# Kernel optimization log

Measured on AMD Instinct MI355X. Metric: run time of the kernel, lower is better.

The kernel has to match this reference:

```python
import jax, jax.numpy as jnp
import numpy as np

NUM_RANKS = 8   # tp_group.size()
M = 8192        # global token dim (batch*seq), M % (256*NUM_RANKS) == 0
N = 4096        # output features
K_LOCAL = 512   # per-rank shard of the contracted dim (global K = 4096)


def setup_inputs() -> dict:
    key = jax.random.key(0)
    k1, k2 = jax.random.split(key)
    # a[r] = this rank's input shard [M, K_local]
    a = jax.random.normal(k1, (NUM_RANKS, M, K_LOCAL), dtype=jnp.float32)
    # b[r] = this rank's weight shard [N, K_local]; GEMM is input @ weight.T
    b = jax.random.normal(k2, (NUM_RANKS, N, K_LOCAL), dtype=jnp.float32)
    return {"a": a, "b": b}


def reference(a, b):
    # Simulates gemm_rs_intra_node across all ranks.
    # Per-rank GEMM (non-transposed weight path: C_r = a_r @ b_r^T)
    R, M_, _ = a.shape
    N_ = b.shape[1]
    m_per_rank = M_ // R
    partial = jnp.einsum('rmk,rnk->rmn', a, b)  # [R, M, N] partial products
    # Reduce-scatter over the M dim: out[r] = sum_src partial[src, r*mpr:(r+1)*mpr, :]
    # (the fused scatter writes each M-chunk into the owning rank's buffer,
    #  kernel_consumer_reduce then sums over source ranks)
    out = partial.reshape(R, R, m_per_rank, N_).sum(axis=0)  # sum over source ranks
    return out  # [R, M_per_rank, N]
```

## Files before the change

kernel.cpp:

```cpp
#include <hip/hip_runtime.h>
#include <hip/hip_bf16.h>
#include <stdint.h>

#define NUM_RANKS 8
#define M_DIM 8192
#define N_DIM 4096
#define K_LOC 512
#define K_DIM 4096
#define NT    (K_DIM / 64)

typedef __bf16 bf16x8 __attribute__((ext_vector_type(8)));
typedef float f32x4 __attribute__((ext_vector_type(4)));

__device__ __forceinline__ uint32_t f2bf(float f) {
    union { float f; uint32_t u; } cv;
    cv.f = f;
    uint32_t x = cv.u;
    return ((x + 0x7fffu + ((x >> 16) & 1u)) >> 16) & 0xffffu;
}

__global__ __launch_bounds__(256) void cvt_fused(
    const float* __restrict__ a, const float* __restrict__ b,
    unsigned short* __restrict__ Abf, unsigned short* __restrict__ Bbf)
{
    const long ACH = (long)NUM_RANKS * M_DIM * (K_LOC / 8);
    const long TCH = ACH + (long)NUM_RANKS * N_DIM * (K_LOC / 8);
    for (long c = (long)blockIdx.x * 256 + threadIdx.x; c < TCH;
         c += (long)gridDim.x * 256) {
        const float* in; unsigned short* out; long e; int rowShift;
        if (c < ACH) { in = a; out = Abf; e = c << 3;        rowShift = 13; }
        else         { in = b; out = Bbf; e = (c - ACH) << 3; rowShift = 12; }
        const int src = (int)(e >> (rowShift + 9));
        const int row = (int)((e >> 9) & ((1 << rowShift) - 1));
        const int k   = (int)(e & 511);
        const float4 f0 = *(const float4*)(in + e);
        const float4 f1 = *(const float4*)(in + e + 4);
        uint4 v;
        v.x = f2bf(f0.x) | (f2bf(f0.y) << 16);
        v.y = f2bf(f0.z) | (f2bf(f0.w) << 16);
        v.z = f2bf(f1.x) | (f2bf(f1.y) << 16);
        v.w = f2bf(f1.z) | (f2bf(f1.w) << 16);
        *(uint4*)(out + ((long)row << 12) + (src << 9) + k) = v;
    }
}

__device__ __forceinline__ void load_lds16(const void* g, void* l) {
    __builtin_amdgcn_global_load_lds(
        (__attribute__((address_space(1))) void*)g,
        (__attribute__((address_space(3))) void*)l,
        16, 0, 0);
}


#define MFMA16 __builtin_amdgcn_mfma_f32_16x16x32_bf16
#define BAR() do { \
    __builtin_amdgcn_sched_barrier(0); \
    asm volatile("s_barrier" ::: "memory"); \
    __builtin_amdgcn_sched_barrier(0); \
} while (0)
#define WAIT_LGKM() do { \
    asm volatile("s_waitcnt lgkmcnt(0)" ::: "memory"); \
    __builtin_amdgcn_sched_barrier(0); \
} while (0)
#define WAIT_VM(n) asm volatile("s_waitcnt vmcnt(" #n ")" ::: "memory")

#define STAGE_A(h, kt, bsel) do { \
    const long kof_ = (long)(kt) * 64; \
    load_lds16(gA0 + (long)((h) * 128) * K_DIM + kof_, \
               lA + (bsel) * 16384 + (h) * 8192); \
    load_lds16(gA0 + (long)((h) * 128 + 64) * K_DIM + kof_, \
               lA + (bsel) * 16384 + (h) * 8192 + 4096); \
} while (0)
#define STAGE_B(h, kt, bsel) do { \
    const long kof_ = (long)(kt) * 64; \
    load_lds16(gB0 + (long)((h) * 128) * K_DIM + kof_, \
               lB + (bsel) * 16384 + (h) * 8192); \
    load_lds16(gB0 + (long)((h) * 128 + 64) * K_DIM + kof_, \
               lB + (bsel) * 16384 + (h) * 8192 + 4096); \
} while (0)

#define READ_A(mh, bsel) do { \
    _Pragma("unroll") \
    for (int mi_ = 0; mi_ < 4; ++mi_) { \
        af[mi_][0] = *(const bf16x8*)(&sA[bsel][baseA0 + ((mh) * 64 + mi_ * 16) * 64]); \
        af[mi_][1] = *(const bf16x8*)(&sA[bsel][baseA1 + ((mh) * 64 + mi_ * 16) * 64]); \
    } \
} while (0)
#define READ_B(nh, bsel) do { \
    _Pragma("unroll") \
    for (int ni_ = 0; ni_ < 2; ++ni_) { \
        bfr[ni_][0] = *(const bf16x8*)(&sB[bsel][baseB0 + ((nh) * 32 + ni_ * 16) * 64]); \
        bfr[ni_][1] = *(const bf16x8*)(&sB[bsel][baseB1 + ((nh) * 32 + ni_ * 16) * 64]); \
    } \
} while (0)

#define DO_MFMA(mh, nh) do { \
    __builtin_amdgcn_s_setprio(1); \
    _Pragma("unroll") \
    for (int mi_ = 0; mi_ < 4; ++mi_) { \
        _Pragma("unroll") \
        for (int ni_ = 0; ni_ < 2; ++ni_) { \
            acc[(mh) * 4 + mi_][(nh) * 2 + ni_] = MFMA16( \
                af[mi_][0], bfr[ni_][0], acc[(mh) * 4 + mi_][(nh) * 2 + ni_], 0, 0, 0); \
            acc[(mh) * 4 + mi_][(nh) * 2 + ni_] = MFMA16( \
                af[mi_][1], bfr[ni_][1], acc[(mh) * 4 + mi_][(nh) * 2 + ni_], 0, 0, 0); \
        } \
    } \
    __builtin_amdgcn_s_setprio(0); \
} while (0)

#define TILE(bsel, kt, sN, sA2, vmend) do { \
    READ_A(0, bsel); READ_B(0, bsel); \
    if (sN) STAGE_A(1, (kt) + 1, (bsel) ^ 1); \
    BAR(); WAIT_LGKM(); DO_MFMA(0, 0); BAR(); \
    READ_B(1, bsel); \
    if (sN) STAGE_B(0, (kt) + 1, (bsel) ^ 1); \
    BAR(); WAIT_LGKM(); DO_MFMA(0, 1); BAR(); \
    READ_A(1, bsel); \
    if (sN) STAGE_B(1, (kt) + 1, (bsel) ^ 1); \
    BAR(); WAIT_LGKM(); DO_MFMA(1, 1); BAR(); \
    READ_B(0, bsel); \
    if (sA2) STAGE_A(0, (kt) + 2, bsel); \
    BAR(); WAIT_LGKM(); DO_MFMA(1, 0); \
    if ((vmend) == 2) { WAIT_VM(2); } \
    else if ((vmend) == 0) { WAIT_VM(0); } \
    BAR(); \
} while (0)

__global__ __launch_bounds__(512, 2) void gemm_bt(
    const unsigned short* __restrict__ A,
    const unsigned short* __restrict__ B,
    float* __restrict__ C)
{
    __shared__ unsigned short sA[2][16384];
    __shared__ unsigned short sB[2][16384];

    const int t    = threadIdx.x;
    const int lane = t & 63;
    const int w    = t >> 6;
    const int wm   = w >> 2;
    const int wn   = w & 3;
    const int l16  = lane & 15;
    const int quad = lane >> 4;

    const int m0 = blockIdx.y << 8;
    const int n0 = blockIdx.x << 8;

    const int r0 = t >> 3;
    const int cs = (((t & 7) ^ ((t >> 3) & 7)) << 3);
    const unsigned short* gA0 = A + (long)(m0 + r0) * K_DIM + cs;
    const unsigned short* gB0 = B + (long)(n0 + r0) * K_DIM + cs;
    unsigned short* lA = &sA[0][t * 8];
    unsigned short* lB = &sB[0][t * 8];

    const int xq = l16 & 7;
    const int baseA0 = ((wm * 128 + l16) << 6) + ((quad ^ xq) << 3);
    const int baseA1 = ((wm * 128 + l16) << 6) + (((4 + quad) ^ xq) << 3);
    const int baseB0 = ((wn * 64 + l16) << 6) + ((quad ^ xq) << 3);
    const int baseB1 = ((wn * 64 + l16) << 6) + (((4 + quad) ^ xq) << 3);

    f32x4 acc[8][4];
#pragma unroll
    for (int i = 0; i < 8; ++i)
#pragma unroll
        for (int j = 0; j < 4; ++j)
            acc[i][j] = (f32x4){0.f, 0.f, 0.f, 0.f};

    bf16x8 af[4][2], bfr[2][2];

    STAGE_A(0, 0, 0); STAGE_A(1, 0, 0); STAGE_B(0, 0, 0); STAGE_B(1, 0, 0);
    STAGE_A(0, 1, 1);
    WAIT_VM(2);
    BAR();

    for (int tt = 0; tt < NT / 2 - 1; ++tt) {
        TILE(0, 2 * tt,     1, 1, 2);
        TILE(1, 2 * tt + 1, 1, 1, 2);
    }
    TILE(0, NT - 2, 1, 0, 0);
    TILE(1, NT - 1, 0, 0, -1);

#pragma unroll
    for (int mi8 = 0; mi8 < 8; ++mi8) {
#pragma unroll
        for (int ni = 0; ni < 4; ++ni) {
            const int col = n0 + wn * 64 + ni * 16 + l16;
            const long rbase = (long)(m0 + wm * 128 + mi8 * 16 + quad * 4);
#pragma unroll
            for (int r = 0; r < 4; ++r)
                C[(rbase + r) * N_DIM + col] = acc[mi8][ni][r];
        }
    }
}

extern "C" void kernel_launch(void* const* d_in, const int* in_sizes, int n_in,
                              void* d_out, int out_size, void* d_ws, size_t ws_size,
                              hipStream_t stream)
{
    const float* a = (const float*)d_in[0];
    const float* b = (const float*)d_in[1];
    float* out = (float*)d_out;

    unsigned short* Abf = (unsigned short*)d_ws;
    unsigned short* Bbf = Abf + (size_t)M_DIM * K_DIM;

    cvt_fused<<<2048, 256, 0, stream>>>(a, b, Abf, Bbf);

    dim3 grid(N_DIM / 256, M_DIM / 256);
    gemm_bt<<<grid, 512, 0, stream>>>(Abf, Bbf, out);
}
```

Baseline: 528.0 us.

## Double-buffer LDS fragment registers and relax waitcnts to overlap reads with MFMA

Restructures the per-tile schedule so LDS fragment reads for the next quarter-tile (and the next tile's first A/B fragments) are issued before the current MFMA block. Waits become partial lgkmcnt counts instead of full drains, and fewer barriers are used. Global-to-LDS staging is reordered so more loads stay in flight, with B staged two tiles ahead. The extra fragment registers raise VGPR pressure, and the reordered stage and barrier timing risks LDS read/write races.

```diff
diff --git a/kernel.cpp b/kernel.cpp
--- a/kernel.cpp
+++ b/kernel.cpp
@@ -58,11 +58,14 @@
     asm volatile("s_barrier" ::: "memory"); \
     __builtin_amdgcn_sched_barrier(0); \
 } while (0)
-#define WAIT_LGKM() do { \
-    asm volatile("s_waitcnt lgkmcnt(0)" ::: "memory"); \
+#define LGKM(n) do { \
+    asm volatile("s_waitcnt lgkmcnt(" #n ")" ::: "memory"); \
     __builtin_amdgcn_sched_barrier(0); \
 } while (0)
-#define WAIT_VM(n) asm volatile("s_waitcnt vmcnt(" #n ")" ::: "memory")
+#define VM_6    asm volatile("s_waitcnt vmcnt(6)" ::: "memory")
+#define VM_2    asm volatile("s_waitcnt vmcnt(2)" ::: "memory")
+#define VM_0    asm volatile("s_waitcnt vmcnt(0)" ::: "memory")
+#define VM_NONE
 
 #define STAGE_A(h, kt, bsel) do { \
     const long kof_ = (long)(kt) * 64; \
@@ -79,51 +82,54 @@
                lB + (bsel) * 16384 + (h) * 8192 + 4096); \
 } while (0)
 
-#define READ_A(mh, bsel) do { \
+#define RD_A(mh, dst, bsel) do { \
     _Pragma("unroll") \
     for (int mi_ = 0; mi_ < 4; ++mi_) { \
-        af[mi_][0] = *(const bf16x8*)(&sA[bsel][baseA0 + ((mh) * 64 + mi_ * 16) * 64]); \
-        af[mi_][1] = *(const bf16x8*)(&sA[bsel][baseA1 + ((mh) * 64 + mi_ * 16) * 64]); \
+        af[dst][mi_][0] = *(const bf16x8*)(&sA[bsel][baseA0 + ((mh) * 64 + mi_ * 16) * 64]); \
+        af[dst][mi_][1] = *(const bf16x8*)(&sA[bsel][baseA1 + ((mh) * 64 + mi_ * 16) * 64]); \
     } \
 } while (0)
-#define READ_B(nh, bsel) do { \
+#define RD_B(nh, dst, bsel) do { \
     _Pragma("unroll") \
     for (int ni_ = 0; ni_ < 2; ++ni_) { \
-        bfr[ni_][0] = *(const bf16x8*)(&sB[bsel][baseB0 + ((nh) * 32 + ni_ * 16) * 64]); \
-        bfr[ni_][1] = *(const bf16x8*)(&sB[bsel][baseB1 + ((nh) * 32 + ni_ * 16) * 64]); \
+        bq[dst][ni_][0] = *(const bf16x8*)(&sB[bsel][baseB0 + ((nh) * 32 + ni_ * 16) * 64]); \
+        bq[dst][ni_][1] = *(const bf16x8*)(&sB[bsel][baseB1 + ((nh) * 32 + ni_ * 16) * 64]); \
     } \
 } while (0)
 
-#define DO_MFMA(mh, nh) do { \
+#define DO_MFMA(mh, nh, aset, bset) do { \
     __builtin_amdgcn_s_setprio(1); \
     _Pragma("unroll") \
     for (int mi_ = 0; mi_ < 4; ++mi_) { \
         _Pragma("unroll") \
         for (int ni_ = 0; ni_ < 2; ++ni_) { \
             acc[(mh) * 4 + mi_][(nh) * 2 + ni_] = MFMA16( \
-                af[mi_][0], bfr[ni_][0], acc[(mh) * 4 + mi_][(nh) * 2 + ni_], 0, 0, 0); \
+                af[aset][mi_][0], bq[bset][ni_][0], \
+                acc[(mh) * 4 + mi_][(nh) * 2 + ni_], 0, 0, 0); \
             acc[(mh) * 4 + mi_][(nh) * 2 + ni_] = MFMA16( \
-                af[mi_][1], bfr[ni_][1], acc[(mh) * 4 + mi_][(nh) * 2 + ni_], 0, 0, 0); \
+                af[aset][mi_][1], bq[bset][ni_][1], \
+                acc[(mh) * 4 + mi_][(nh) * 2 + ni_], 0, 0, 0); \
         } \
     } \
     __builtin_amdgcn_s_setprio(0); \
 } while (0)
 
-#define TILE(bsel, kt, sN, sA2, vmend) do { \
-    READ_A(0, bsel); READ_B(0, bsel); \
-    if (sN) STAGE_A(1, (kt) + 1, (bsel) ^ 1); \
-    BAR(); WAIT_LGKM(); DO_MFMA(0, 0); BAR(); \
-    READ_B(1, bsel); \
-    if (sN) STAGE_B(0, (kt) + 1, (bsel) ^ 1); \
-    BAR(); WAIT_LGKM(); DO_MFMA(0, 1); BAR(); \
-    READ_A(1, bsel); \
-    if (sN) STAGE_B(1, (kt) + 1, (bsel) ^ 1); \
-    BAR(); WAIT_LGKM(); DO_MFMA(1, 1); BAR(); \
-    READ_B(0, bsel); \
-    if (sA2) STAGE_A(0, (kt) + 2, bsel); \
-    BAR(); WAIT_LGKM(); DO_MFMA(1, 0); \
-    if ((vmend) == 2) { WAIT_VM(2); } \
-    else if ((vmend) == 0) { WAIT_VM(0); } \
+#define TILE(bsel, kt, sP1, sP3, sP4, e1, VMA) do { \
+     \
+    RD_B(1, 2, bsel); \
+    if (sP1) STAGE_A(1, (kt) + 1, (bsel) ^ 1); \
+    LGKM(4);  DO_MFMA(0, 0, 0, bsel);  BAR(); \
+     \
+    RD_A(1, 1, bsel); \
+    LGKM(8);  DO_MFMA(0, 1, 0, 2);     BAR(); \
+     \
+    if (sP3) STAGE_B(0, (kt) + 2, bsel); \
+    LGKM(0);  DO_MFMA(1, 1, 1, 2); \
+    VMA;  BAR(); \
+     \
+    if (e1) { RD_A(0, 0, (bsel) ^ 1); RD_B(0, (bsel) ^ 1, (bsel) ^ 1); } \
+    if (sP4) { STAGE_A(0, (kt) + 2, bsel); STAGE_B(1, (kt) + 2, bsel); } \
+    DO_MFMA(1, 0, 1, bsel); \
     BAR(); \
 } while (0)
 
@@ -166,19 +172,21 @@
         for (int j = 0; j < 4; ++j)
             acc[i][j] = (f32x4){0.f, 0.f, 0.f, 0.f};
 
-    bf16x8 af[4][2], bfr[2][2];
+    bf16x8 af[2][4][2];
+    bf16x8 bq[3][2][2];
 
     STAGE_A(0, 0, 0); STAGE_A(1, 0, 0); STAGE_B(0, 0, 0); STAGE_B(1, 0, 0);
-    STAGE_A(0, 1, 1);
-    WAIT_VM(2);
+    STAGE_B(0, 1, 1); STAGE_A(0, 1, 1); STAGE_B(1, 1, 1);
+    VM_6;
     BAR();
+    RD_A(0, 0, 0); RD_B(0, 0, 0);
 
     for (int tt = 0; tt < NT / 2 - 1; ++tt) {
-        TILE(0, 2 * tt,     1, 1, 2);
-        TILE(1, 2 * tt + 1, 1, 1, 2);
+        TILE(0, 2 * tt,     1, 1, 1, 1, VM_2);
+        TILE(1, 2 * tt + 1, 1, 1, 1, 1, VM_2);
     }
-    TILE(0, NT - 2, 1, 0, 0);
-    TILE(1, NT - 1, 0, 0, -1);
+    TILE(0, NT - 2, 1, 0, 0, 1, VM_0);
+    TILE(1, NT - 1, 0, 0, 0, 0, VM_NONE);
 
 #pragma unroll
     for (int mi8 = 0; mi8 < 8; ++mi8) {
```

Measured after the change: 497.7 us. -5.7%, faster.
